# Kernel optimization log

Measured on AMD Instinct MI355X. Metric: run time of the kernel, lower is better.

## Reference

```python
import jax, jax.numpy as jnp
import numpy as np

B, L, D = 1, 4096, 1024
H, HD = 16, 64

def setup_inputs() -> dict:
    key = jax.random.key(0)
    ks = jax.random.split(key, 5)
    scale = 1.0 / np.sqrt(D)
    return {
        "x": jax.random.normal(ks[0], (B, L, D), dtype=jnp.float32),
        "Wq": jax.random.normal(ks[1], (D, D), dtype=jnp.float32) * scale,
        "Wk": jax.random.normal(ks[2], (D, D), dtype=jnp.float32) * scale,
        "Wv": jax.random.normal(ks[3], (D, D), dtype=jnp.float32) * scale,
        "Wo": jax.random.normal(ks[4], (D, D), dtype=jnp.float32) * scale,
    }

def reference(x, Wq, Wk, Wv, Wo):
    Bc, Lc, _ = x.shape
    # torch Linear: y = x @ W.T
    q = (x @ Wq.T).reshape(Bc, Lc, H, HD).transpose(0, 2, 1, 3)  # [B,H,L,hd]
    k = (x @ Wk.T).reshape(Bc, Lc, H, HD).transpose(0, 2, 1, 3)
    v = (x @ Wv.T).reshape(Bc, Lc, H, HD).transpose(0, 2, 1, 3)
    scale = HD ** -0.5
    scores = jnp.einsum('bhqd,bhkd->bhqk', q, k) * scale  # [B,H,L,L]
    causal = jnp.tril(jnp.ones((Lc, Lc), dtype=bool))
    scores = jnp.where(causal, scores, -jnp.inf)
    attn = jax.nn.softmax(scores, axis=-1)
    out = jnp.einsum('bhqk,bhkd->bhqd', attn, v)
    out = out.transpose(0, 2, 1, 3).reshape(Bc, Lc, H * HD)
    return out @ Wo.T
```

## Files before the change

kernel.cpp:

```cpp
#include <hip/hip_runtime.h>
#include <hip/hip_bf16.h>
#include <stdint.h>

#define L_SEQ   4096
#define D_MODEL 1024
#define N_HEADS 16
#define HEAD_DIM 64

typedef uint16_t u16;
typedef __bf16 bf16x8 __attribute__((ext_vector_type(8)));
typedef short s16x4 __attribute__((ext_vector_type(4)));
typedef float floatx4 __attribute__((ext_vector_type(4)));

__device__ __forceinline__ floatx4 mfma32(bf16x8 a, bf16x8 b, floatx4 c) {
  return __builtin_amdgcn_mfma_f32_16x16x32_bf16(a, b, c, 0, 0, 0);
}

__device__ __forceinline__ floatx4 mfma16(s16x4 a, s16x4 b, floatx4 c) {
#if __has_builtin(__builtin_amdgcn_mfma_f32_16x16x16bf16_1k)
  return __builtin_amdgcn_mfma_f32_16x16x16bf16_1k(a, b, c, 0, 0, 0);
#else
  floatx4 d;
  asm volatile("v_mfma_f32_16x16x16_bf16 %0, %1, %2, %3"
               : "=v"(d) : "v"(a), "v"(b), "v"(c));
  return d;
#endif
}

__device__ __forceinline__ float hw_exp2(float x) {
  return __builtin_amdgcn_exp2f(x);
}

__device__ __forceinline__ uint32_t fbits(float f) {
  union { float f; uint32_t u; } x; x.f = f; return x.u;
}

__device__ __forceinline__ uint32_t pack_bf16_trunc(float f1, float f0) {
  return __builtin_amdgcn_perm(fbits(f1), fbits(f0), 0x07060302u);
}

__device__ __forceinline__ void load16_lds(const u16* g, u16* l) {
  __builtin_amdgcn_global_load_lds(
      (const __attribute__((address_space(1))) void*)g,
      (__attribute__((address_space(3))) void*)l, 16, 0, 0);
}

__device__ __forceinline__ u16 f2bf(float f) {
  uint32_t u = fbits(f);
  uint32_t r = u + 0x7FFFu + ((u >> 16) & 1u);
  return (u16)(r >> 16);
}

#define Q_PRESCALE 0.18033688011112042f

__global__ __launch_bounds__(256) void cvt_kernel(
    const float* __restrict__ x,  const float* __restrict__ wq,
    const float* __restrict__ wk, const float* __restrict__ wv,
    const float* __restrict__ wo,
    u16* __restrict__ xb, u16* __restrict__ wqb, u16* __restrict__ wkb,
    u16* __restrict__ wvb, u16* __restrict__ wob) {
  const int z = blockIdx.z;
  const float* s; u16* d; int n;
  if (z == 0)      { s = x;  d = xb;  n = L_SEQ * D_MODEL; }
  else if (z == 1) { s = wq; d = wqb; n = D_MODEL * D_MODEL; }
  else if (z == 2) { s = wk; d = wkb; n = D_MODEL * D_MODEL; }
  else if (z == 3) { s = wv; d = wvb; n = D_MODEL * D_MODEL; }
  else             { s = wo; d = wob; n = D_MODEL * D_MODEL; }
  const int stride = gridDim.x * 256 * 4;
  for (int i = (blockIdx.x * 256 + threadIdx.x) * 4; i < n; i += stride) {
    float4 v = *(const float4*)(s + i);
    ushort4 o;
    o.x = f2bf(v.x); o.y = f2bf(v.y); o.z = f2bf(v.z); o.w = f2bf(v.w);
    *(ushort4*)(d + i) = o;
  }
}

__global__ __launch_bounds__(256) void qkv_gemm_kernel(
    const u16* __restrict__ X,
    const u16* __restrict__ Wq, const u16* __restrict__ Wk, const u16* __restrict__ Wv,
    u16* __restrict__ Qo, u16* __restrict__ Ko, u16* __restrict__ VTo) {
  constexpr int BK = 32, Kdim = D_MODEL, NIT = Kdim / BK;
  __shared__ __align__(16) u16 As[2][128 * BK];
  __shared__ __align__(16) u16 Bs[2][128 * BK];

  const int b = blockIdx.x;
  const int g = b & 7, i2 = b >> 3;
  const int z = i2 % 3, j = i2 / 3;
  const int x = (g & 3) * 8 + (j & 7);
  const int y = (g >> 2) * 4 + (j >> 3);

  const u16* __restrict__ A;
  const u16* __restrict__ B;
  int m0, n0;
  if (z < 2) { A = X; B = z ? Wk : Wq; m0 = x * 128; n0 = y * 128; }
  else       { A = Wv; B = X;          m0 = y * 128; n0 = x * 128; }

  const int tid = threadIdx.x;
  const int wave = tid >> 6, lane = tid & 63;
  const int wm = wave & 1, wn = wave >> 1;
  const int quad = lane >> 4, l15 = lane & 15;

  floatx4 acc[4][4] = {};

  const int cbase = wave * 128;
  const int c0 = cbase + lane, c1 = c0 + 64;
  const int r0 = c0 >> 2, cc0 = (c0 & 3) * 8;
  const int r1 = c1 >> 2, cc1 = (c1 & 3) * 8;

  auto stage = [&](int k0, int sel) {
    load16_lds(&A[(size_t)(m0 + r0) * Kdim + k0 + cc0], &As[sel][cbase * 8]);
    load16_lds(&A[(size_t)(m0 + r1) * Kdim + k0 + cc1], &As[sel][(cbase + 64) * 8]);
    load16_lds(&B[(size_t)(n0 + r0) * Kdim + k0 + cc0], &Bs[sel][cbase * 8]);
    load16_lds(&B[(size_t)(n0 + r1) * Kdim + k0 + cc1], &Bs[sel][(cbase + 64) * 8]);
  };

  stage(0, 0);
  for (int kk = 0; kk < NIT; ++kk) {
    __syncthreads();
    if (kk + 1 < NIT) stage((kk + 1) * BK, (kk + 1) & 1);
    const u16* Asc = As[kk & 1];
    const u16* Bsc = Bs[kk & 1];

    bf16x8 af[4], wf[4];
#pragma unroll
    for (int i = 0; i < 4; ++i)
      af[i] = *(const bf16x8*)(&Asc[(wm * 64 + i * 16 + l15) * BK + quad * 8]);
#pragma unroll
    for (int jn = 0; jn < 4; ++jn)
      wf[jn] = *(const bf16x8*)(&Bsc[(wn * 64 + jn * 16 + l15) * BK + quad * 8]);
#pragma unroll
    for (int i = 0; i < 4; ++i)
#pragma unroll
      for (int jn = 0; jn < 4; ++jn)
        acc[i][jn] = mfma32(af[i], wf[jn], acc[i][jn]);
  }

  const float scale = (z == 0) ? Q_PRESCALE : 1.0f;
  u16* __restrict__ C = (z == 0) ? Qo : (z == 1) ? Ko : VTo;
#pragma unroll
  for (int i = 0; i < 4; ++i) {
    const int mb = m0 + wm * 64 + i * 16 + quad * 4;
#pragma unroll
    for (int jn = 0; jn < 4; ++jn) {
      const int n = n0 + wn * 64 + jn * 16 + l15;
#pragma unroll
      for (int r = 0; r < 4; ++r) {
        const int m = mb + r;
        if (z < 2) {
          C[(size_t)(n >> 6) * (size_t)L_SEQ * HEAD_DIM + (size_t)m * HEAD_DIM + (n & 63)] =
              f2bf(acc[i][jn][r] * scale);
        } else {
          C[(size_t)(m >> 6) * (size_t)L_SEQ * HEAD_DIM + (size_t)(m & 63) * L_SEQ + n] =
              f2bf(acc[i][jn][r]);
        }
      }
    }
  }
}

__global__ __launch_bounds__(256) void out_gemm_kernel(
    const u16* __restrict__ A, const u16* __restrict__ W, float* __restrict__ C) {
  constexpr int BK = 32, Kdim = D_MODEL, NIT = Kdim / BK;
  __shared__ __align__(16) u16 As[2][128 * BK];
  __shared__ __align__(16) u16 Bs[2][64 * BK];

  const int tid = threadIdx.x;
  const int wave = tid >> 6, lane = tid & 63;
  const int wm = wave & 1, wn = wave >> 1;
  const int quad = lane >> 4, l15 = lane & 15;
  const int m0 = blockIdx.x * 128, n0 = blockIdx.y * 64;

  floatx4 acc[4][2] = {};

  const int cbase = wave * 128;
  const int c0 = cbase + lane, c1 = c0 + 64;
  const int ra0 = c0 >> 2, ca0 = (c0 & 3) * 8;
  const int ra1 = c1 >> 2, ca1 = (c1 & 3) * 8;
  const int cb = wave * 64 + lane;
  const int rb = cb >> 2, cbcol = (cb & 3) * 8;

  auto stage = [&](int k0, int sel) {
    load16_lds(&A[(size_t)(m0 + ra0) * Kdim + k0 + ca0], &As[sel][cbase * 8]);
    load16_lds(&A[(size_t)(m0 + ra1) * Kdim + k0 + ca1], &As[sel][(cbase + 64) * 8]);
    load16_lds(&W[(size_t)(n0 + rb) * Kdim + k0 + cbcol], &Bs[sel][wave * 64 * 8]);
  };

  stage(0, 0);
  for (int kk = 0; kk < NIT; ++kk) {
    __syncthreads();
    if (kk + 1 < NIT) stage((kk + 1) * BK, (kk + 1) & 1);
    const u16* Asc = As[kk & 1];
    const u16* Bsc = Bs[kk & 1];

    bf16x8 af[4], wf[2];
#pragma unroll
    for (int i = 0; i < 4; ++i)
      af[i] = *(const bf16x8*)(&Asc[(wm * 64 + i * 16 + l15) * BK + quad * 8]);
#pragma unroll
    for (int jn = 0; jn < 2; ++jn)
      wf[jn] = *(const bf16x8*)(&Bsc[(wn * 32 + jn * 16 + l15) * BK + quad * 8]);
#pragma unroll
    for (int i = 0; i < 4; ++i)
#pragma unroll
      for (int jn = 0; jn < 2; ++jn)
        acc[i][jn] = mfma32(af[i], wf[jn], acc[i][jn]);
  }

#pragma unroll
  for (int i = 0; i < 4; ++i) {
    const int mb = m0 + wm * 64 + i * 16 + quad * 4;
#pragma unroll
    for (int jn = 0; jn < 2; ++jn) {
      const int n = n0 + wn * 32 + jn * 16 + l15;
#pragma unroll
      for (int r = 0; r < 4; ++r)
        C[(size_t)(mb + r) * D_MODEL + n] = acc[i][jn][r];
    }
  }
}

#define LDP 72
__global__ __launch_bounds__(256, 3) void attn_kernel(
    const u16* __restrict__ Q, const u16* __restrict__ K,
    const u16* __restrict__ VT, u16* __restrict__ Oa) {
  __shared__ __align__(16) u16 Vts[2][64 * LDP];
  __shared__ __align__(16) float Of[4 * 64 * 16];
  __shared__ float Lf[4 * 64 + 64];

  const int b = blockIdx.x;
  const int h = (b & 7) * 2 + (b >> 8);
  const int pair = (b >> 3) & 31;
  const int tid = threadIdx.x;
  const int wave = tid >> 6, lane = tid & 63;
  const int quad = lane >> 4, l15 = lane & 15;

  const size_t hoff = (size_t)h * L_SEQ * HEAD_DIM;
  const u16* __restrict__ Qh = Q + hoff;
  const u16* __restrict__ Kh = K + hoff;
  const u16* __restrict__ VTh = VT + hoff;

  const u16* const Kg = Kh + (size_t)(wave * 16 + l15) * HEAD_DIM;
  const int vd0 = lane >> 1, vk = (lane & 1) * 8;
  const int vofs0 = vd0 * LDP + wave * 16 + vk;
  const int vofs1 = (vd0 + 32) * LDP + wave * 16 + vk;
  const u16* const Vg0 = VTh + (size_t)vd0 * L_SEQ + wave * 16 + vk;
  const u16* const Vg1 = VTh + (size_t)(vd0 + 32) * L_SEQ + wave * 16 + vk;
  const int vread = wave * 16 + quad * 4;

  for (int half = 0; half < 2; ++half) {
    const int qt = half ? (63 - pair) : pair;
    const int q0 = qt * 64;

    bf16x8 qf[4][2];
#pragma unroll
    for (int jq = 0; jq < 4; ++jq) {
      const u16* qrow = Qh + (size_t)(q0 + jq * 16 + l15) * HEAD_DIM;
      qf[jq][0] = *(const bf16x8*)(qrow + quad * 8);
      qf[jq][1] = *(const bf16x8*)(qrow + 32 + quad * 8);
    }

    floatx4 oacc[4][4] = {};
    float psum[4] = {};

    float4 va  = *(const float4*)(Vg0);
    float4 vb4 = *(const float4*)(Vg1);
    *(float4*)(&Vts[0][vofs0]) = va;
    *(float4*)(&Vts[0][vofs1]) = vb4;
    if (qt > 0) {
      va  = *(const float4*)(Vg0 + 64);
      vb4 = *(const float4*)(Vg1 + 64);
    }
    bf16x8 kc0 = *(const bf16x8*)(Kg + quad * 8);
    bf16x8 kc1 = *(const bf16x8*)(Kg + 32 + quad * 8);

    for (int kt = 0; kt <= qt; ++kt) {
      const u16* Vc = Vts[kt & 1];
      s16x4 vb[4];
#pragma unroll
      for (int nt = 0; nt < 4; ++nt)
        vb[nt] = *(const s16x4*)(&Vc[(nt * 16 + l15) * LDP + vread]);

      if (kt < qt) {
        u16* Vn = Vts[(kt + 1) & 1];
        *(float4*)(&Vn[vofs0]) = va;
        *(float4*)(&Vn[vofs1]) = vb4;
        if (kt + 1 < qt) {
          va  = *(const float4*)(Vg0 + (size_t)(kt + 2) * 64);
          vb4 = *(const float4*)(Vg1 + (size_t)(kt + 2) * 64);
        }
      }
      bf16x8 kf0 = kc0, kf1 = kc1;
      if (kt < qt) {
        const u16* Kn = Kg + (size_t)(kt + 1) * 64 * HEAD_DIM;
        kc0 = *(const bf16x8*)(Kn + quad * 8);
        kc1 = *(const bf16x8*)(Kn + 32 + quad * 8);
      }

      floatx4 s[4];
#pragma unroll
      for (int jq = 0; jq < 4; ++jq) {
        floatx4 z = {};
        z = mfma32(kf0, qf[jq][0], z);
        z = mfma32(kf1, qf[jq][1], z);
        s[jq] = z;
      }

      if (kt == qt) {
        const int keyw = wave * 16 + quad * 4;
#pragma unroll
        for (int jq = 0; jq < 4; ++jq) {
          const int qloc = jq * 16 + l15;
#pragma unroll
          for (int r = 0; r < 4; ++r)
            if (keyw + r > qloc) s[jq][r] = -1e30f;
        }
      }

      s16x4 pa[4];
#pragma unroll
      for (int jq = 0; jq < 4; ++jq) {
        float p0 = hw_exp2(s[jq][0]);
        float p1 = hw_exp2(s[jq][1]);
        float p2 = hw_exp2(s[jq][2]);
        float p3 = hw_exp2(s[jq][3]);
        psum[jq] += (p0 + p1) + (p2 + p3);
        union { uint32_t w[2]; s16x4 v; } pu;
        pu.w[0] = pack_bf16_trunc(p1, p0);
        pu.w[1] = pack_bf16_trunc(p3, p2);
        pa[jq] = pu.v;
      }

#pragma unroll
      for (int jq = 0; jq < 4; ++jq)
#pragma unroll
        for (int nt = 0; nt < 4; ++nt)
          oacc[jq][nt] = mfma16(pa[jq], vb[nt], oacc[jq][nt]);
    }

#pragma unroll
    for (int jq = 0; jq < 4; ++jq) {
      psum[jq] += __shfl_xor(psum[jq], 16, 64);
      psum[jq] += __shfl_xor(psum[jq], 32, 64);
    }
    if (quad == 0) {
#pragma unroll
      for (int jq = 0; jq < 4; ++jq)
        Lf[wave * 64 + jq * 16 + l15] = psum[jq];
    }
    __syncthreads();
    if (tid < 64) {
      float lt = Lf[tid] + Lf[64 + tid] + Lf[128 + tid] + Lf[192 + tid];
      Lf[256 + tid] = 1.0f / lt;
    }

    const int qc = tid >> 2, d4 = (tid & 3) * 4;
#pragma unroll
    for (int nt = 0; nt < 4; ++nt) {
#pragma unroll
      for (int jq = 0; jq < 4; ++jq)
#pragma unroll
        for (int r = 0; r < 4; ++r)
          Of[wave * 1024 + (jq * 16 + quad * 4 + r) * 16 + l15] = oacc[jq][nt][r];
      __syncthreads();
      const float invq = Lf[256 + qc];
      floatx4 a0 = *(const floatx4*)&Of[0 * 1024 + qc * 16 + d4];
      floatx4 a1 = *(const floatx4*)&Of[1 * 1024 + qc * 16 + d4];
      floatx4 a2 = *(const floatx4*)&Of[2 * 1024 + qc * 16 + d4];
      floatx4 a3 = *(const floatx4*)&Of[3 * 1024 + qc * 16 + d4];
      floatx4 sum = (a0 + a1) + (a2 + a3);
      ushort4 o;
      o.x = f2bf(sum[0] * invq); o.y = f2bf(sum[1] * invq);
      o.z = f2bf(sum[2] * invq); o.w = f2bf(sum[3] * invq);
      *(ushort4*)(Oa + (size_t)(q0 + qc) * D_MODEL + (size_t)h * HEAD_DIM +
                  nt * 16 + d4) = o;
      __syncthreads();
    }
  }
}

extern "C" void kernel_launch(void* const* d_in, const int* in_sizes, int n_in,
                              void* d_out, int out_size, void* d_ws, size_t ws_size,
                              hipStream_t stream) {
  const float* x  = (const float*)d_in[0];
  const float* Wq = (const float*)d_in[1];
  const float* Wk = (const float*)d_in[2];
  const float* Wv = (const float*)d_in[3];
  const float* Wo = (const float*)d_in[4];
  float* out = (float*)d_out;

  const size_t XN = (size_t)L_SEQ * D_MODEL;
  const size_t WN = (size_t)D_MODEL * D_MODEL;
  const size_t HLHD = (size_t)N_HEADS * L_SEQ * HEAD_DIM;

  u16* x_bf  = (u16*)d_ws;
  u16* wq_bf = x_bf + XN;
  u16* wk_bf = wq_bf + WN;
  u16* wv_bf = wk_bf + WN;
  u16* wo_bf = wv_bf + WN;
  u16* q_ws  = wo_bf + WN;
  u16* k_ws  = q_ws + HLHD;
  u16* vT_ws = k_ws + HLHD;
  u16* a_ws  = vT_ws + HLHD;

  dim3 gc(1024, 1, 5);
  cvt_kernel<<<gc, 256, 0, stream>>>(x, Wq, Wk, Wv, Wo,
                                     x_bf, wq_bf, wk_bf, wv_bf, wo_bf);

  dim3 gqkv(768, 1, 1);
  qkv_gemm_kernel<<<gqkv, 256, 0, stream>>>(x_bf, wq_bf, wk_bf, wv_bf,
                                            q_ws, k_ws, vT_ws);

  dim3 ga(512, 1, 1);
  attn_kernel<<<ga, 256, 0, stream>>>(q_ws, k_ws, vT_ws, a_ws);

  dim3 go(L_SEQ / 128, D_MODEL / 64, 1);
  out_gemm_kernel<<<go, 256, 0, stream>>>(a_ws, wo_bf, out);
}
```

Measured before the change: 195.7 us.

## Process 128-key tiles with 16x16x32 MFMA, async V loads to LDS, one q-tile per block

Restructures the attention kernel so each block handles one query tile, with heaviest tiles scheduled first, instead of pairing tiles per block. The launch grid grows from 512 to 1024 blocks. Each iteration now covers two 64-key chunks, so the P·V product can use the wider 16x16x32 bf16 MFMA instead of 16x16x16. V is streamed straight from global memory into double-buffered LDS with global_load_lds and explicit vmcnt waits, replacing register staging plus LDS stores, and the V buffers share LDS with the output reduction buffer through a union. This is meant to cut instruction and LDS-store overhead and improve latency hiding, but it relies on hand-counted waitcnt ordering and no per-iteration barrier.

Result: slower. 226.5 us (+15.8%).

```diff
diff --git a/kernel.cpp b/kernel.cpp
--- a/kernel.cpp
+++ b/kernel.cpp
@@ -14,17 +14,6 @@
 
 __device__ __forceinline__ floatx4 mfma32(bf16x8 a, bf16x8 b, floatx4 c) {
   return __builtin_amdgcn_mfma_f32_16x16x32_bf16(a, b, c, 0, 0, 0);
-}
-
-__device__ __forceinline__ floatx4 mfma16(s16x4 a, s16x4 b, floatx4 c) {
-#if __has_builtin(__builtin_amdgcn_mfma_f32_16x16x16bf16_1k)
-  return __builtin_amdgcn_mfma_f32_16x16x16bf16_1k(a, b, c, 0, 0, 0);
-#else
-  floatx4 d;
-  asm volatile("v_mfma_f32_16x16x16_bf16 %0, %1, %2, %3"
-               : "=v"(d) : "v"(a), "v"(b), "v"(c));
-  return d;
-#endif
 }
 
 __device__ __forceinline__ float hw_exp2(float x) {
@@ -219,17 +208,18 @@
   }
 }
 
-#define LDP 72
 __global__ __launch_bounds__(256, 3) void attn_kernel(
     const u16* __restrict__ Q, const u16* __restrict__ K,
     const u16* __restrict__ VT, u16* __restrict__ Oa) {
-  __shared__ __align__(16) u16 Vts[2][64 * LDP];
-  __shared__ __align__(16) float Of[4 * 64 * 16];
+  __shared__ __align__(16) union SMem {
+    u16 V[4][4][64 * 16];
+    float Of[4 * 64 * 16];
+  } sm;
   __shared__ float Lf[4 * 64 + 64];
 
   const int b = blockIdx.x;
-  const int h = (b & 7) * 2 + (b >> 8);
-  const int pair = (b >> 3) & 31;
+  const int h = b & 15;
+  const int qt = 63 - (b >> 4);
   const int tid = threadIdx.x;
   const int wave = tid >> 6, lane = tid & 63;
   const int quad = lane >> 4, l15 = lane & 15;
@@ -239,142 +229,144 @@
   const u16* __restrict__ Kh = K + hoff;
   const u16* __restrict__ VTh = VT + hoff;
 
+  const int q0 = qt * 64;
+  const int np = (qt + 2) >> 1;
+
   const u16* const Kg = Kh + (size_t)(wave * 16 + l15) * HEAD_DIM;
-  const int vd0 = lane >> 1, vk = (lane & 1) * 8;
-  const int vofs0 = vd0 * LDP + wave * 16 + vk;
-  const int vofs1 = (vd0 + 32) * LDP + wave * 16 + vk;
-  const u16* const Vg0 = VTh + (size_t)vd0 * L_SEQ + wave * 16 + vk;
-  const u16* const Vg1 = VTh + (size_t)(vd0 + 32) * L_SEQ + wave * 16 + vk;
-  const int vread = wave * 16 + quad * 4;
-
-  for (int half = 0; half < 2; ++half) {
-    const int qt = half ? (63 - pair) : pair;
-    const int q0 = qt * 64;
-
-    bf16x8 qf[4][2];
+  const u16* const Vsrc =
+      VTh + (size_t)(lane >> 1) * L_SEQ + wave * 16 + (lane & 1) * 8;
+  u16* const Vdst = &sm.V[0][0][0] + wave * 1024;
+
+  bf16x8 qf[4][2];
+#pragma unroll
+  for (int jq = 0; jq < 4; ++jq) {
+    const u16* qrow = Qh + (size_t)(q0 + jq * 16 + l15) * HEAD_DIM;
+    qf[jq][0] = *(const bf16x8*)(qrow + quad * 8);
+    qf[jq][1] = *(const bf16x8*)(qrow + 32 + quad * 8);
+  }
+
+  floatx4 oacc[4][4] = {};
+  float psum[4] = {};
+
+  load16_lds(Vsrc,                           Vdst);
+  load16_lds(Vsrc + (size_t)32 * L_SEQ,      Vdst + 512);
+  load16_lds(Vsrc + 64,                      Vdst + 4096);
+  load16_lds(Vsrc + 64 + (size_t)32 * L_SEQ, Vdst + 4096 + 512);
+  bf16x8 k00 = *(const bf16x8*)(Kg + quad * 8);
+  bf16x8 k01 = *(const bf16x8*)(Kg + 32 + quad * 8);
+  bf16x8 k10 = *(const bf16x8*)(Kg + (size_t)64 * HEAD_DIM + quad * 8);
+  bf16x8 k11 = *(const bf16x8*)(Kg + (size_t)64 * HEAD_DIM + 32 + quad * 8);
+
+  union PB { uint32_t w[4]; bf16x8 v; };
+
+  for (int pt = 0; pt < np; ++pt) {
+    asm volatile("s_waitcnt vmcnt(4)" ::: "memory");
+
+    const u16* Va = &sm.V[(pt & 1) * 2][wave][0];
+    const u16* Vb = Va + 4096;
+    PB vf[4];
+#pragma unroll
+    for (int nt = 0; nt < 4; ++nt) {
+      const int o = nt * 256 + l15 * 16 + quad * 4;
+      uint2 lo = *(const uint2*)(Va + o);
+      uint2 hi = *(const uint2*)(Vb + o);
+      vf[nt].w[0] = lo.x; vf[nt].w[1] = lo.y;
+      vf[nt].w[2] = hi.x; vf[nt].w[3] = hi.y;
+    }
+
+    if (pt + 1 < np) {
+      const u16* src = Vsrc + (size_t)(pt + 1) * 128;
+      u16* dst = Vdst + ((pt + 1) & 1) * 2 * 4096;
+      load16_lds(src,                           dst);
+      load16_lds(src + (size_t)32 * L_SEQ,      dst + 512);
+      load16_lds(src + 64,                      dst + 4096);
+      load16_lds(src + 64 + (size_t)32 * L_SEQ, dst + 4096 + 512);
+    }
+
+    const bool lastp = (pt == np - 1);
+    const int kb = pt * 128 + wave * 16 + quad * 4;
+
 #pragma unroll
     for (int jq = 0; jq < 4; ++jq) {
-      const u16* qrow = Qh + (size_t)(q0 + jq * 16 + l15) * HEAD_DIM;
-      qf[jq][0] = *(const bf16x8*)(qrow + quad * 8);
-      qf[jq][1] = *(const bf16x8*)(qrow + 32 + quad * 8);
-    }
-
-    floatx4 oacc[4][4] = {};
-    float psum[4] = {};
-
-    float4 va  = *(const float4*)(Vg0);
-    float4 vb4 = *(const float4*)(Vg1);
-    *(float4*)(&Vts[0][vofs0]) = va;
-    *(float4*)(&Vts[0][vofs1]) = vb4;
-    if (qt > 0) {
-      va  = *(const float4*)(Vg0 + 64);
-      vb4 = *(const float4*)(Vg1 + 64);
-    }
-    bf16x8 kc0 = *(const bf16x8*)(Kg + quad * 8);
-    bf16x8 kc1 = *(const bf16x8*)(Kg + 32 + quad * 8);
-
-    for (int kt = 0; kt <= qt; ++kt) {
-      const u16* Vc = Vts[kt & 1];
-      s16x4 vb[4];
-#pragma unroll
-      for (int nt = 0; nt < 4; ++nt)
-        vb[nt] = *(const s16x4*)(&Vc[(nt * 16 + l15) * LDP + vread]);
-
-      if (kt < qt) {
-        u16* Vn = Vts[(kt + 1) & 1];
-        *(float4*)(&Vn[vofs0]) = va;
-        *(float4*)(&Vn[vofs1]) = vb4;
-        if (kt + 1 < qt) {
-          va  = *(const float4*)(Vg0 + (size_t)(kt + 2) * 64);
-          vb4 = *(const float4*)(Vg1 + (size_t)(kt + 2) * 64);
+      floatx4 s0 = {}, s1 = {};
+      s0 = mfma32(k00, qf[jq][0], s0);
+      s0 = mfma32(k01, qf[jq][1], s0);
+      s1 = mfma32(k10, qf[jq][0], s1);
+      s1 = mfma32(k11, qf[jq][1], s1);
+
+      if (lastp) {
+        const int qg = q0 + jq * 16 + l15;
+#pragma unroll
+        for (int r = 0; r < 4; ++r) {
+          if (kb + r > qg)      s0[r] = -1e30f;
+          if (kb + 64 + r > qg) s1[r] = -1e30f;
         }
       }
-      bf16x8 kf0 = kc0, kf1 = kc1;
-      if (kt < qt) {
-        const u16* Kn = Kg + (size_t)(kt + 1) * 64 * HEAD_DIM;
-        kc0 = *(const bf16x8*)(Kn + quad * 8);
-        kc1 = *(const bf16x8*)(Kn + 32 + quad * 8);
-      }
-
-      floatx4 s[4];
-#pragma unroll
-      for (int jq = 0; jq < 4; ++jq) {
-        floatx4 z = {};
-        z = mfma32(kf0, qf[jq][0], z);
-        z = mfma32(kf1, qf[jq][1], z);
-        s[jq] = z;
-      }
-
-      if (kt == qt) {
-        const int keyw = wave * 16 + quad * 4;
-#pragma unroll
-        for (int jq = 0; jq < 4; ++jq) {
-          const int qloc = jq * 16 + l15;
-#pragma unroll
-          for (int r = 0; r < 4; ++r)
-            if (keyw + r > qloc) s[jq][r] = -1e30f;
-        }
-      }
-
-      s16x4 pa[4];
-#pragma unroll
-      for (int jq = 0; jq < 4; ++jq) {
-        float p0 = hw_exp2(s[jq][0]);
-        float p1 = hw_exp2(s[jq][1]);
-        float p2 = hw_exp2(s[jq][2]);
-        float p3 = hw_exp2(s[jq][3]);
-        psum[jq] += (p0 + p1) + (p2 + p3);
-        union { uint32_t w[2]; s16x4 v; } pu;
-        pu.w[0] = pack_bf16_trunc(p1, p0);
-        pu.w[1] = pack_bf16_trunc(p3, p2);
-        pa[jq] = pu.v;
-      }
-
-#pragma unroll
-      for (int jq = 0; jq < 4; ++jq)
-#pragma unroll
-        for (int nt = 0; nt < 4; ++nt)
-          oacc[jq][nt] = mfma16(pa[jq], vb[nt], oacc[jq][nt]);
-    }
-
-#pragma unroll
-    for (int jq = 0; jq < 4; ++jq) {
-      psum[jq] += __shfl_xor(psum[jq], 16, 64);
-      psum[jq] += __shfl_xor(psum[jq], 32, 64);
-    }
-    if (quad == 0) {
-#pragma unroll
-      for (int jq = 0; jq < 4; ++jq)
-        Lf[wave * 64 + jq * 16 + l15] = psum[jq];
-    }
+
+      float p0 = hw_exp2(s0[0]), p1 = hw_exp2(s0[1]);
+      float p2 = hw_exp2(s0[2]), p3 = hw_exp2(s0[3]);
+      float r0 = hw_exp2(s1[0]), r1 = hw_exp2(s1[1]);
+      float r2 = hw_exp2(s1[2]), r3 = hw_exp2(s1[3]);
+      psum[jq] += ((p0 + p1) + (p2 + p3)) + ((r0 + r1) + (r2 + r3));
+
+      PB pa;
+      pa.w[0] = pack_bf16_trunc(p1, p0);
+      pa.w[1] = pack_bf16_trunc(p3, p2);
+      pa.w[2] = pack_bf16_trunc(r1, r0);
+      pa.w[3] = pack_bf16_trunc(r3, r2);
+
+#pragma unroll
+      for (int nt = 0; nt < 4; ++nt)
+        oacc[jq][nt] = mfma32(pa.v, vf[nt].v, oacc[jq][nt]);
+    }
+
+    if (pt + 1 < np) {
+      asm volatile("" ::: "memory");
+      const u16* kp = Kg + (size_t)(pt + 1) * 128 * HEAD_DIM;
+      k00 = *(const bf16x8*)(kp + quad * 8);
+      k01 = *(const bf16x8*)(kp + 32 + quad * 8);
+      k10 = *(const bf16x8*)(kp + (size_t)64 * HEAD_DIM + quad * 8);
+      k11 = *(const bf16x8*)(kp + (size_t)64 * HEAD_DIM + 32 + quad * 8);
+    }
+  }
+
+#pragma unroll
+  for (int jq = 0; jq < 4; ++jq) {
+    psum[jq] += __shfl_xor(psum[jq], 16, 64);
+    psum[jq] += __shfl_xor(psum[jq], 32, 64);
+  }
+  if (quad == 0) {
+#pragma unroll
+    for (int jq = 0; jq < 4; ++jq)
+      Lf[wave * 64 + jq * 16 + l15] = psum[jq];
+  }
+  __syncthreads();
+  if (tid < 64) {
+    float lt = Lf[tid] + Lf[64 + tid] + Lf[128 + tid] + Lf[192 + tid];
+    Lf[256 + tid] = 1.0f / lt;
+  }
+
+  const int qc = tid >> 2, d4 = (tid & 3) * 4;
+#pragma unroll
+  for (int nt = 0; nt < 4; ++nt) {
+#pragma unroll
+    for (int jq = 0; jq < 4; ++jq)
+#pragma unroll
+      for (int r = 0; r < 4; ++r)
+        sm.Of[wave * 1024 + (jq * 16 + quad * 4 + r) * 16 + l15] = oacc[jq][nt][r];
     __syncthreads();
-    if (tid < 64) {
-      float lt = Lf[tid] + Lf[64 + tid] + Lf[128 + tid] + Lf[192 + tid];
-      Lf[256 + tid] = 1.0f / lt;
-    }
-
-    const int qc = tid >> 2, d4 = (tid & 3) * 4;
-#pragma unroll
-    for (int nt = 0; nt < 4; ++nt) {
-#pragma unroll
-      for (int jq = 0; jq < 4; ++jq)
-#pragma unroll
-        for (int r = 0; r < 4; ++r)
-          Of[wave * 1024 + (jq * 16 + quad * 4 + r) * 16 + l15] = oacc[jq][nt][r];
-      __syncthreads();
-      const float invq = Lf[256 + qc];
-      floatx4 a0 = *(const floatx4*)&Of[0 * 1024 + qc * 16 + d4];
-      floatx4 a1 = *(const floatx4*)&Of[1 * 1024 + qc * 16 + d4];
-      floatx4 a2 = *(const floatx4*)&Of[2 * 1024 + qc * 16 + d4];
-      floatx4 a3 = *(const floatx4*)&Of[3 * 1024 + qc * 16 + d4];
-      floatx4 sum = (a0 + a1) + (a2 + a3);
-      ushort4 o;
-      o.x = f2bf(sum[0] * invq); o.y = f2bf(sum[1] * invq);
-      o.z = f2bf(sum[2] * invq); o.w = f2bf(sum[3] * invq);
-      *(ushort4*)(Oa + (size_t)(q0 + qc) * D_MODEL + (size_t)h * HEAD_DIM +
-                  nt * 16 + d4) = o;
-      __syncthreads();
-    }
+    const float invq = Lf[256 + qc];
+    floatx4 a0 = *(const floatx4*)&sm.Of[0 * 1024 + qc * 16 + d4];
+    floatx4 a1 = *(const floatx4*)&sm.Of[1 * 1024 + qc * 16 + d4];
+    floatx4 a2 = *(const floatx4*)&sm.Of[2 * 1024 + qc * 16 + d4];
+    floatx4 a3 = *(const floatx4*)&sm.Of[3 * 1024 + qc * 16 + d4];
+    floatx4 sum = (a0 + a1) + (a2 + a3);
+    ushort4 o;
+    o.x = f2bf(sum[0] * invq); o.y = f2bf(sum[1] * invq);
+    o.z = f2bf(sum[2] * invq); o.w = f2bf(sum[3] * invq);
+    *(ushort4*)(Oa + (size_t)(q0 + qc) * D_MODEL + (size_t)h * HEAD_DIM +
+                nt * 16 + d4) = o;
+    __syncthreads();
   }
 }
 
@@ -410,7 +402,7 @@
   qkv_gemm_kernel<<<gqkv, 256, 0, stream>>>(x_bf, wq_bf, wk_bf, wv_bf,
                                             q_ws, k_ws, vT_ws);
 
-  dim3 ga(512, 1, 1);
+  dim3 ga(1024, 1, 1);
   attn_kernel<<<ga, 256, 0, stream>>>(q_ws, k_ws, vT_ws, a_ws);
 
   dim3 go(L_SEQ / 128, D_MODEL / 64, 1);
```
